# Kernel optimization log

Measured on AMD Instinct MI355X. Metric: run time of the kernel, lower is better.

## Reference

```python
import jax, jax.numpy as jnp
import numpy as np

D_MODEL = 256
D_INNER = 512   # expand=2 * d_model
D_STATE = 16
D_CONV = 4
DT_RANK = 16    # ceil(d_model/16)
N_BLOCKS = 5
BATCH = 8192
INPUT_DIM = 2048
NUM_CLASSES = 8


def setup_inputs() -> dict:
    key = jax.random.key(0)
    ks = jax.random.split(key, 10)
    rn = lambda k, shape, s: jax.random.normal(k, shape, jnp.float32) * s
    inp = {}
    inp['x'] = rn(ks[0], (BATCH, INPUT_DIM), 1.0)
    # preprocess Linear(input_dim, 256)
    inp['W_pre'] = rn(ks[1], (D_MODEL, INPUT_DIM), 0.02)
    inp['b_pre'] = jnp.zeros((D_MODEL,), jnp.float32)
    # per-block Mamba params, stacked over N_BLOCKS
    inp['in_proj_w'] = rn(ks[2], (N_BLOCKS, 2 * D_INNER, D_MODEL), 0.02)
    inp['conv_w'] = rn(ks[3], (N_BLOCKS, D_INNER, 1, D_CONV), 0.1)   # depthwise, groups=d_inner
    inp['conv_b'] = jnp.zeros((N_BLOCKS, D_INNER), jnp.float32)
    inp['x_proj_w'] = rn(ks[4], (N_BLOCKS, DT_RANK + 2 * D_STATE, D_INNER), 0.02)
    inp['dt_proj_w'] = rn(ks[5], (N_BLOCKS, D_INNER, DT_RANK), 0.1)
    inp['dt_proj_b'] = rn(ks[6], (N_BLOCKS, D_INNER), 0.1)
    # S4D-real init: A = 1..d_state, A_log = log(A)
    A = jnp.tile(jnp.arange(1, D_STATE + 1, dtype=jnp.float32)[None, None, :], (N_BLOCKS, D_INNER, 1))
    inp['A_log'] = jnp.log(A)
    inp['D'] = jnp.ones((N_BLOCKS, D_INNER), jnp.float32)
    inp['out_proj_w'] = rn(ks[7], (N_BLOCKS, D_MODEL, D_INNER), 0.02)
    inp['ln_g'] = jnp.ones((D_MODEL,), jnp.float32)
    inp['ln_b'] = jnp.zeros((D_MODEL,), jnp.float32)
    inp['W_cls'] = rn(ks[8], (NUM_CLASSES, D_MODEL), 0.02)
    inp['b_cls'] = jnp.zeros((NUM_CLASSES,), jnp.float32)
    return inp


def _mamba(x, in_w, cw, cb, xw, dtw, dtb, Alog, Dp, ow):
    # x: (B, L, d_model)
    B, L, _ = x.shape
    xz = jnp.einsum('bld,ed->ble', x, in_w)            # (B, L, 2*d_inner)
    xi, z = jnp.split(xz, 2, axis=-1)
    # causal depthwise conv1d over the sequence axis
    xt = xi.transpose(0, 2, 1)                         # (B, d_inner, L)
    xc = jax.lax.conv_general_dilated(
        xt, cw, window_strides=(1,), padding=[(D_CONV - 1, 0)],
        dimension_numbers=('NCH', 'OIH', 'NCH'), feature_group_count=D_INNER)
    xi = jax.nn.silu((xc + cb[None, :, None]).transpose(0, 2, 1))   # (B, L, d_inner)
    xdbl = jnp.einsum('bld,ed->ble', xi, xw)           # (B, L, dt_rank + 2*d_state)
    dt, Bm, Cm = jnp.split(xdbl, [DT_RANK, DT_RANK + D_STATE], axis=-1)
    dt = jax.nn.softplus(jnp.einsum('blr,dr->bld', dt, dtw) + dtb)  # (B, L, d_inner)
    A = -jnp.exp(Alog)                                  # (d_inner, d_state)
    dA = jnp.exp(dt[..., None] * A)                     # (B, L, d_inner, d_state)
    dBx = dt[..., None] * Bm[:, :, None, :] * xi[..., None]

    def step(h, t):
        dA_t, dBx_t, C_t = t
        h = dA_t * h + dBx_t                            # (B, d_inner, d_state)
        return h, jnp.einsum('bds,bs->bd', h, C_t)

    h0 = jnp.zeros((B, D_INNER, D_STATE), x.dtype)
    _, ys = jax.lax.scan(step, h0, (dA.swapaxes(0, 1), dBx.swapaxes(0, 1), Cm.swapaxes(0, 1)))
    y = ys.swapaxes(0, 1) + xi * Dp                     # (B, L, d_inner)
    y = y * jax.nn.silu(z)
    return jnp.einsum('bld,ed->ble', y, ow)             # (B, L, d_model)


def reference(x, W_pre, b_pre, in_proj_w, conv_w, conv_b, x_proj_w, dt_proj_w,
              dt_proj_b, A_log, D, out_proj_w, ln_g, ln_b, W_cls, b_cls):
    # dropout is identity in eval mode
    h = (x @ W_pre.T + b_pre)[:, None, :]               # (B, 1, 256)
    for i in range(N_BLOCKS):
        h = h + _mamba(h, in_proj_w[i], conv_w[i], conv_b[i], x_proj_w[i],
                       dt_proj_w[i], dt_proj_b[i], A_log[i], D[i], out_proj_w[i])
    mu = h.mean(-1, keepdims=True)
    var = ((h - mu) ** 2).mean(-1, keepdims=True)
    hn = (h - mu) * jax.lax.rsqrt(var + 1e-5) * ln_g + ln_b
    return hn[:, 0, :] @ W_cls.T + b_cls                # (B, num_classes)
```

## Files before the change

### kernel.cpp

```cpp
#include <hip/hip_runtime.h>
#include <hip/hip_bf16.h>

typedef __attribute__((ext_vector_type(8))) short bf16x8;
typedef __attribute__((ext_vector_type(4))) short s16x4;
typedef __attribute__((ext_vector_type(4))) float f32x4;
typedef __attribute__((ext_vector_type(4))) float float4v;

static __device__ __forceinline__ unsigned short f2b(float f) {
  unsigned int u = __builtin_bit_cast(unsigned int, f);
  u += 0x7fffu + ((u >> 16) & 1u);
  return (unsigned short)(u >> 16);
}
static __device__ __forceinline__ float b2f(unsigned short s) {
  unsigned int u = ((unsigned int)s) << 16;
  return __builtin_bit_cast(float, u);
}
static __device__ __forceinline__ float fsilu(float x) {
  float e = __builtin_amdgcn_exp2f(-1.44269504f * x);
  return x * __builtin_amdgcn_rcpf(1.f + e);
}
static __device__ __forceinline__ float fsoftplus(float a) {
  if (a > 20.f) return a;
  float t = __builtin_amdgcn_exp2f(1.44269504f * a);
  return 0.69314718f * __builtin_amdgcn_logf(1.f + t);
}
static __device__ __forceinline__ void gl16(const void* g, void* l) {
  __builtin_amdgcn_global_load_lds(
      (const __attribute__((address_space(1))) unsigned int*)g,
      (__attribute__((address_space(3))) unsigned int*)l, 16, 0, 0);
}
template <int N>
static __device__ __forceinline__ void waitv() {
  if constexpr (N == 0) asm volatile("s_waitcnt vmcnt(0)" ::: "memory");
  else if constexpr (N == 2) asm volatile("s_waitcnt vmcnt(2)" ::: "memory");
  else if constexpr (N == 4) asm volatile("s_waitcnt vmcnt(4)" ::: "memory");
  else if constexpr (N == 6) asm volatile("s_waitcnt vmcnt(6)" ::: "memory");
  else if constexpr (N == 8) asm volatile("s_waitcnt vmcnt(8)" ::: "memory");
}
static __device__ __forceinline__ void lgkm_bar() {
  asm volatile("s_waitcnt lgkmcnt(0)" ::: "memory");
  __builtin_amdgcn_s_barrier();
}

template <int TM, int TN>
__global__ __launch_bounds__(256) void gemm_pl(
    const unsigned short* __restrict__ A, const unsigned short* __restrict__ W,
    int N, int K, int GY,
    const float* __restrict__ p0, float* __restrict__ of,
    unsigned short* __restrict__ ob) {
  constexpr int FM = TM / 32, FN = TN / 32;
  constexpr int IA = TM / 64, IW = TN / 64;
  constexpr int LPT = IA + IW;
  __shared__ __align__(16) unsigned short As[4][TM * 32];
  __shared__ __align__(16) unsigned short Ws[4][TN * 32];

  const int t = threadIdx.x, lane = t & 63, wave = t >> 6;
  const int lr = lane & 15;
  const int q = gridDim.x >> 3;
  const int s = (blockIdx.x & 7) * q + (blockIdx.x >> 3);
  const int bm = (s / GY) * TM, bn = (s % GY) * TN;
  const int wr = (wave >> 1) * (TM / 2), wc = (wave & 1) * (TN / 2);

  f32x4 acc[FM][FN];
#pragma unroll
  for (int i = 0; i < FM; ++i)
#pragma unroll
    for (int j = 0; j < FN; ++j) acc[i][j] = (f32x4){0.f, 0.f, 0.f, 0.f};

  const unsigned short* agB =
      A + (long)(bm + wave * (TM / 4) + (lane >> 2)) * K +
      ((lane & 3) ^ ((lane >> 3) & 3)) * 8;
  const unsigned short* wgB =
      W + (long)(bn + wave * (TN / 4) + (lane >> 2)) * K +
      ((lane & 3) ^ ((lane >> 3) & 3)) * 8;

  auto STAGE = [&](int k0, int b) {
#pragma unroll
    for (int j = 0; j < IA; ++j)
      gl16(agB + k0 + (long)j * 16 * K, &As[b][(wave * (TM / 4) + j * 16) * 32]);
#pragma unroll
    for (int j = 0; j < IW; ++j)
      gl16(wgB + k0 + (long)j * 16 * K, &Ws[b][(wave * (TN / 4) + j * 16) * 32]);
  };

  auto COMPUTE = [&](int b) {
    bf16x8 af[FM], bg[FN];
    const int sw = ((lane >> 4) ^ ((lane >> 1) & 3)) * 8;
#pragma unroll
    for (int m = 0; m < FM; ++m)
      af[m] = *(const bf16x8*)&As[b][(wr + m * 16 + lr) * 32 + sw];
#pragma unroll
    for (int n = 0; n < FN; ++n)
      bg[n] = *(const bf16x8*)&Ws[b][(wc + n * 16 + lr) * 32 + sw];
    __builtin_amdgcn_s_setprio(1);
#pragma unroll
    for (int m = 0; m < FM; ++m)
#pragma unroll
      for (int n = 0; n < FN; ++n)
        acc[m][n] = __builtin_amdgcn_mfma_f32_16x16x32_bf16(af[m], bg[n],
                                                            acc[m][n], 0, 0, 0);
    __builtin_amdgcn_s_setprio(0);
  };

  const int NT = K >> 5;
  STAGE(0, 0);
  STAGE(32, 1);
  for (int tt = 0; tt < NT; ++tt) {
    if (tt + 2 < NT) {
      STAGE((tt + 2) << 5, (tt + 2) & 3);
      waitv<2 * LPT>();
    } else if (tt + 1 < NT) {
      waitv<LPT>();
    } else {
      waitv<0>();
    }
    __builtin_amdgcn_s_barrier();
    COMPUTE(tt & 3);
    __builtin_amdgcn_sched_barrier(0);
  }

  const int m0 = bm + wr + (lane >> 4) * 4;
  const int n0 = bn + wc + lr;
#pragma unroll
  for (int mi = 0; mi < FM; ++mi)
#pragma unroll
    for (int ni = 0; ni < FN; ++ni) {
      const int n = n0 + ni * 16;
#pragma unroll
      for (int r = 0; r < 4; ++r) {
        const int m = m0 + mi * 16 + r;
        float v = acc[mi][ni][r] + p0[n];
        of[(long)m * N + n] = v;
        ob[(long)m * N + n] = f2b(v);
      }
    }
}

__global__ __launch_bounds__(512) void mamba5(
    const unsigned short* __restrict__ hb0, const float* __restrict__ h0,
    const unsigned short* __restrict__ inwb,
    const unsigned short* __restrict__ xwpb,
    const unsigned short* __restrict__ dtwpb,
    const unsigned short* __restrict__ owb,
    const float* __restrict__ conv_b, const float* __restrict__ dt_b,
    const float* __restrict__ Dp, float* __restrict__ hout) {
  __shared__ __align__(16) unsigned short SMEM[81216];
  unsigned short* XiL = SMEM;
  unsigned short* SzL = SMEM + 16384;
  unsigned short* Ring = SMEM + 32768;
  unsigned short* HLr = SMEM + 65536;
  float* Dxl = (float*)(SMEM + 73728);
  float* BCl = (float*)(SMEM + 78080);
  float* Par = (float*)(SMEM + 78144);

  const int t = threadIdx.x, lane = t & 63, w = t >> 6;
  const int lr = lane & 15, lg = lane >> 4;
  const int bm = blockIdx.x * 32;
  const int fm = w & 1, fn = w >> 1;
  const int arow = fm * 16 + lr;
  const int br = fn * 16 + lr;
  const int m0 = fm * 16 + lg * 4;

#pragma unroll
  for (int j = 0; j < 2; ++j) {
    const int i = w * 2 + j;
    const int row = 2 * i + (lane >> 5);
    const int c = (lane & 31) ^ (row & 7);
    gl16(hb0 + (long)(bm + row) * 256 + c * 8, HLr + i * 512);
  }
  float hres[4][4];
#pragma unroll
  for (int ng = 0; ng < 4; ++ng)
#pragma unroll
    for (int r = 0; r < 4; ++r)
      hres[ng][r] = h0[(long)(bm + m0 + r) * 256 + ng * 64 + fn * 16 + lr];
  waitv<0>();
  __builtin_amdgcn_s_barrier();

  for (int blk = 0; blk < 5; ++blk) {
    const unsigned short* inw = inwb + (long)blk * 1024 * 256;
    const unsigned short* xwp = xwpb + (long)blk * 64 * 512;
    const unsigned short* dtwp = dtwpb + (long)blk * 512 * 32;
    const unsigned short* ow = owb + (long)blk * 256 * 512;
    const float* cbv = conv_b + blk * 512;
    const float* dtbv = dt_b + blk * 512;
    const float* Dv = Dp + blk * 512;

    auto STAGE1 = [&](int tt, int slot) {
      const int nt = tt >> 1, kh = tt & 1;
#pragma unroll
      for (int j = 0; j < 2; ++j) {
        const int u = w * 2 + j;
        const int row = 4 * u + (lane >> 4);
        const int c = (lane & 15) ^ (row & 7);
        gl16(inw + (long)(nt * 64 + row) * 256 + kh * 128 + c * 8,
             Ring + slot * 8192 + u * 512);
      }
    };
    if (w < 6) {
      const float* ps = (w < 2) ? cbv + (w & 1) * 256
                      : (w < 4) ? dtbv + (w & 1) * 256
                                : Dv + (w & 1) * 256;
      gl16(ps + lane * 4, (unsigned short*)Par + w * 512);
    }
    STAGE1(0, 0); STAGE1(1, 1); STAGE1(2, 2);
    f32x4 acc1 = {0.f, 0.f, 0.f, 0.f};
    for (int tt = 0; tt < 32; ++tt) {
      if (tt + 2 < 32) waitv<4>();
      else if (tt + 1 < 32) waitv<2>();
      else waitv<0>();
      __builtin_amdgcn_s_barrier();
      if (tt + 3 < 32) STAGE1(tt + 3, (tt + 3) & 3);
      __builtin_amdgcn_sched_barrier(0);
      const int nt = tt >> 1, kh = tt & 1;
      const int c = nt * 64 + fn * 16 + lr;
      if (kh == 0) {
        const float cb0 = (c < 512) ? Par[c] : 0.f;
        acc1 = (f32x4){cb0, cb0, cb0, cb0};
      }
      const unsigned short* Bs = Ring + (tt & 3) * 8192;
      {
        bf16x8 af[4], bg[4];
#pragma unroll
        for (int kc = 0; kc < 4; ++kc) {
          af[kc] = *(const bf16x8*)
              &HLr[arow * 256 + ((((kh * 4 + kc) * 4 + lg) ^ (arow & 7)) * 8)];
          bg[kc] = *(const bf16x8*)
              &Bs[br * 128 + (((kc * 4 + lg) ^ (br & 7)) * 8)];
        }
        __builtin_amdgcn_s_setprio(1);
#pragma unroll
        for (int kc = 0; kc < 4; ++kc)
          acc1 = __builtin_amdgcn_mfma_f32_16x16x32_bf16(af[kc], bg[kc], acc1,
                                                         0, 0, 0);
        __builtin_amdgcn_s_setprio(0);
      }
      if (kh == 1) {
        if (c < 512) {
#pragma unroll
          for (int r = 0; r < 4; ++r) {
            const int row = m0 + r;
            XiL[row * 512 + (((c >> 3) ^ (row & 7)) * 8) + (c & 7)] =
                f2b(fsilu(acc1[r]));
          }
        } else {
#pragma unroll
          for (int r = 0; r < 4; ++r)
            SzL[(m0 + r) * 512 + (c - 512)] = f2b(fsilu(acc1[r]));
        }
      }
      __builtin_amdgcn_sched_barrier(0);
    }
    lgkm_bar();

#pragma unroll
    for (int j = 0; j < 8; ++j) {
      const int i = w * 8 + j;
      gl16(xwp + (long)i * 512 + (lane ^ (i & 7)) * 8, Ring + i * 512);
    }
    waitv<0>();
    __builtin_amdgcn_s_barrier();
    {
      f32x4 a2 = {0.f, 0.f, 0.f, 0.f};
      bf16x8 af, bg;
      __builtin_amdgcn_s_setprio(1);
#pragma unroll
      for (int kc = 0; kc < 16; ++kc) {
        af = *(const bf16x8*)
            &XiL[arow * 512 + (((kc * 4 + lg) ^ (arow & 7)) * 8)];
        bg = *(const bf16x8*)
            &Ring[br * 512 + (((kc * 4 + lg) ^ (br & 7)) * 8)];
        a2 = __builtin_amdgcn_mfma_f32_16x16x32_bf16(af, bg, a2, 0, 0, 0);
      }
      __builtin_amdgcn_s_setprio(0);
#pragma unroll
      for (int r = 0; r < 4; ++r) Dxl[(m0 + r) * 68 + fn * 16 + lr] = a2[r];
    }
    lgkm_bar();

#pragma unroll
    for (int j = 0; j < 4; ++j) {
      const int u = w * 4 + j;
      const int row = u * 16 + (lane >> 2);
      const int c = (lane & 3) ^ (row & 3);
      gl16(dtwp + (long)row * 32 + c * 8, Ring + u * 512);
    }
    if (t < 32) {
      float bc = 0.f;
      const float* dx = &Dxl[t * 68];
#pragma unroll
      for (int s2 = 0; s2 < 16; ++s2) bc += dx[16 + s2] * dx[32 + s2];
      BCl[t] = bc;
    }
    bf16x8 afdt;
    {
      const float* dx = &Dxl[arow * 68 + lg * 8];
#pragma unroll
      for (int e = 0; e < 8; ++e) afdt[e] = (short)f2b(dx[e]);
    }
    waitv<0>();
    lgkm_bar();

#pragma unroll
    for (int tt = 0; tt < 8; ++tt) {
      const int d = tt * 64 + fn * 16 + lr;
      bf16x8 bg = *(const bf16x8*)&Ring[d * 32 + ((lg ^ (d & 3)) * 8)];
      f32x4 da = __builtin_amdgcn_mfma_f32_16x16x32_bf16(
          afdt, bg, (f32x4){0.f, 0.f, 0.f, 0.f}, 0, 0, 0);
      const float dbv = Par[512 + d], dvv = Par[1024 + d];
#pragma unroll
      for (int r = 0; r < 4; ++r) {
        const int row = m0 + r;
        const float dtv = fsoftplus(da[r] + dbv);
        const int xoff = row * 512 + (((d >> 3) ^ (row & 7)) * 8) + (d & 7);
        const float y = b2f(XiL[xoff]) * (dtv * BCl[row] + dvv) *
                        b2f(SzL[row * 512 + d]);
        XiL[xoff] = f2b(y);
      }
    }
    lgkm_bar();

    auto STAGE5 = [&](int tt, int slot) {
      const int ng = tt >> 2, kq = tt & 3;
#pragma unroll
      for (int j = 0; j < 2; ++j) {
        const int u = w * 2 + j;
        const int row = u * 4 + (lane >> 4);
        const int c = (lane & 15) ^ (row & 7);
        gl16(ow + (long)(ng * 64 + row) * 512 + kq * 128 + c * 8,
             Ring + slot * 8192 + u * 512);
      }
    };
    STAGE5(0, 0); STAGE5(1, 1); STAGE5(2, 2);
    f32x4 acc5 = {0.f, 0.f, 0.f, 0.f};
    for (int tt = 0; tt < 16; ++tt) {
      if (tt + 2 < 16) waitv<4>();
      else if (tt + 1 < 16) waitv<2>();
      else waitv<0>();
      __builtin_amdgcn_s_barrier();
      if (tt + 3 < 16) STAGE5(tt + 3, (tt + 3) & 3);
      __builtin_amdgcn_sched_barrier(0);
      const int ng = tt >> 2, kq = tt & 3;
      if (kq == 0) acc5 = (f32x4){0.f, 0.f, 0.f, 0.f};
      const unsigned short* Bs = Ring + (tt & 3) * 8192;
      {
        bf16x8 af[4], bg[4];
#pragma unroll
        for (int kc = 0; kc < 4; ++kc) {
          af[kc] = *(const bf16x8*)
              &XiL[arow * 512 + (((kq * 16 + kc * 4 + lg) ^ (arow & 7)) * 8)];
          bg[kc] = *(const bf16x8*)
              &Bs[br * 128 + (((kc * 4 + lg) ^ (br & 7)) * 8)];
        }
        __builtin_amdgcn_s_setprio(1);
#pragma unroll
        for (int kc = 0; kc < 4; ++kc)
          acc5 = __builtin_amdgcn_mfma_f32_16x16x32_bf16(af[kc], bg[kc], acc5,
                                                         0, 0, 0);
        __builtin_amdgcn_s_setprio(0);
      }
      if (kq == 3) {
        const int col = ng * 64 + fn * 16 + lr;
#pragma unroll
        for (int r = 0; r < 4; ++r) {
          const int row = m0 + r;
          const float v = acc5[r] + hres[ng][r];
          hres[ng][r] = v;
          HLr[row * 256 + (((col >> 3) ^ (row & 7)) * 8) + (col & 7)] = f2b(v);
        }
      }
      __builtin_amdgcn_sched_barrier(0);
    }
    lgkm_bar();
  }

#pragma unroll
  for (int ng = 0; ng < 4; ++ng)
#pragma unroll
    for (int r = 0; r < 4; ++r)
      hout[(long)(bm + m0 + r) * 256 + ng * 64 + fn * 16 + lr] = hres[ng][r];
}

__global__ __launch_bounds__(256) void castx(const float* __restrict__ s,
                                             unsigned short* __restrict__ d) {
  const int n4 = (8192 * 2048) / 4;
  for (int i = blockIdx.x * 256 + threadIdx.x; i < n4; i += gridDim.x * 256) {
    float4v v = ((const float4v*)s)[i];
    s16x4 o;
    o[0] = (short)f2b(v[0]); o[1] = (short)f2b(v[1]);
    o[2] = (short)f2b(v[2]); o[3] = (short)f2b(v[3]);
    ((s16x4*)d)[i] = o;
  }
}

__global__ __launch_bounds__(256) void precast(
    const float* __restrict__ wpre, const float* __restrict__ inw,
    const float* __restrict__ ow, const float* __restrict__ xw,
    const float* __restrict__ dtw, const float* __restrict__ cw,
    unsigned short* __restrict__ wpreb, unsigned short* __restrict__ inwb,
    unsigned short* __restrict__ owb, unsigned short* __restrict__ xwpb,
    unsigned short* __restrict__ dtwpb) {
  const int S0 = 524288;
  const int S1 = S0 + 1310720;
  const int S2 = S1 + 655360;
  const int S3 = S2 + 163840;
  const int S4 = S3 + 81920;
  int i4 = (blockIdx.x * 256 + threadIdx.x) * 4;
  if (i4 >= S4) return;
  float4v v = {0.f, 0.f, 0.f, 0.f};
  unsigned short* dst;
  if (i4 < S0) {
    v = *(const float4v*)(wpre + i4);
    dst = wpreb + i4;
  } else if (i4 < S1) {
    int o = i4 - S0;
    v = *(const float4v*)(inw + o);
    int b = o >> 18, row = (o >> 8) & 1023;
    if (row < 512) {
      float c3 = cw[(b * 512 + row) * 4 + 3];
      v[0] *= c3; v[1] *= c3; v[2] *= c3; v[3] *= c3;
    }
    dst = inwb + o;
  } else if (i4 < S2) {
    int o = i4 - S1;
    v = *(const float4v*)(ow + o);
    dst = owb + o;
  } else if (i4 < S3) {
    int o = i4 - S2;
    dst = xwpb + o;
    int k = o & 511, j = (o >> 9) & 63, b = o >> 15;
    if (j < 48) v = *(const float4v*)(xw + ((long)(b * 48 + j)) * 512 + k);
  } else {
    int o = i4 - S3;
    dst = dtwpb + o;
    int k = o & 31, dd = o >> 5;
    if (k < 16) v = *(const float4v*)(dtw + (long)dd * 16 + k);
  }
  s16x4 sv;
  sv[0] = (short)f2b(v[0]); sv[1] = (short)f2b(v[1]);
  sv[2] = (short)f2b(v[2]); sv[3] = (short)f2b(v[3]);
  *(s16x4*)dst = sv;
}

__global__ __launch_bounds__(256) void final_ln_cls(
    const float* __restrict__ h, const float* __restrict__ g,
    const float* __restrict__ be, const float* __restrict__ Wc,
    const float* __restrict__ bc, float* __restrict__ out) {
  const int wave = threadIdx.x >> 6, lane = threadIdx.x & 63;
  const int row = blockIdx.x * 4 + wave;
  const float4v* hr = (const float4v*)(h + (long)row * 256);
  float4v v = hr[lane];
  float s = v[0] + v[1] + v[2] + v[3];
#pragma unroll
  for (int o = 32; o; o >>= 1) s += __shfl_xor(s, o);
  const float mu = s * (1.f / 256.f);
  float d0 = v[0] - mu, d1 = v[1] - mu, d2 = v[2] - mu, d3 = v[3] - mu;
  float qq = d0 * d0 + d1 * d1 + d2 * d2 + d3 * d3;
#pragma unroll
  for (int o = 32; o; o >>= 1) qq += __shfl_xor(qq, o);
  const float rs = rsqrtf(qq * (1.f / 256.f) + 1e-5f);
  const float4v gv = ((const float4v*)g)[lane];
  const float4v bv = ((const float4v*)be)[lane];
  float hn[4];
  hn[0] = d0 * rs * gv[0] + bv[0];
  hn[1] = d1 * rs * gv[1] + bv[1];
  hn[2] = d2 * rs * gv[2] + bv[2];
  hn[3] = d3 * rs * gv[3] + bv[3];
  float lg[8];
#pragma unroll
  for (int o = 0; o < 8; ++o) {
    const float4v wv = ((const float4v*)(Wc + o * 256))[lane];
    float p = hn[0] * wv[0] + hn[1] * wv[1] + hn[2] * wv[2] + hn[3] * wv[3];
#pragma unroll
    for (int x = 32; x; x >>= 1) p += __shfl_xor(p, x);
    lg[o] = p;
  }
  if (lane == 0) {
#pragma unroll
    for (int o = 0; o < 8; ++o) out[(long)row * 8 + o] = lg[o] + bc[o];
  }
}

extern "C" void kernel_launch(void* const* d_in, const int* in_sizes, int n_in,
                              void* d_out, int out_size, void* d_ws,
                              size_t ws_size, hipStream_t stream) {
  const float* x      = (const float*)d_in[0];
  const float* W_pre  = (const float*)d_in[1];
  const float* b_pre  = (const float*)d_in[2];
  const float* in_w   = (const float*)d_in[3];
  const float* conv_w = (const float*)d_in[4];
  const float* conv_b = (const float*)d_in[5];
  const float* x_w    = (const float*)d_in[6];
  const float* dt_w   = (const float*)d_in[7];
  const float* dt_b   = (const float*)d_in[8];
  const float* Dp     = (const float*)d_in[10];
  const float* out_w  = (const float*)d_in[11];
  const float* ln_g   = (const float*)d_in[12];
  const float* ln_b   = (const float*)d_in[13];
  const float* W_cls  = (const float*)d_in[14];
  const float* b_cls  = (const float*)d_in[15];
  float* out = (float*)d_out;

  char* w = (char*)d_ws;
  unsigned short* wpreb = (unsigned short*)w; w += 256 * 2048 * 2;
  unsigned short* inwb  = (unsigned short*)w; w += 5 * 1024 * 256 * 2;
  unsigned short* xwpb  = (unsigned short*)w; w += 5 * 64 * 512 * 2;
  unsigned short* owb   = (unsigned short*)w; w += 5 * 256 * 512 * 2;
  unsigned short* dtwpb = (unsigned short*)w; w += 5 * 512 * 32 * 2;
  float*          h     = (float*)w;          w += 8192 * 256 * 4;
  unsigned short* hb    = (unsigned short*)w; w += 8192 * 256 * 2;
  unsigned short* xb    = (unsigned short*)w; w += 8192 * 2048 * 2;

  precast<<<2672, 256, 0, stream>>>(W_pre, in_w, out_w, x_w, dt_w, conv_w,
                                    wpreb, inwb, owb, xwpb, dtwpb);
  castx<<<2048, 256, 0, stream>>>(x, xb);

  gemm_pl<128, 64><<<256, 256, 0, stream>>>(
      xb, wpreb, 256, 2048, 4, b_pre, h, hb);

  mamba5<<<256, 512, 0, stream>>>(hb, h, inwb, xwpb, dtwpb, owb,
                                  conv_b, dt_b, Dp, h);

  final_ln_cls<<<2048, 256, 0, stream>>>(h, ln_g, ln_b, W_cls, b_cls, out);
}
```

Baseline: 220.7 us.

## Retile in_proj and out_proj GEMMs to 2x2 MFMA fragments per wave with larger stages

Each wave now computes a 32x32 register tile (2x2 MFMA fragments) over full N-chunks of 256 columns instead of one 16x16 fragment. This gives fragment reuse, since each A and B fragment loaded from LDS feeds two MFMAs. Weight staging moves from a 4-slot ring of 64x128 tiles with a prefetch depth of 3 to a double buffer of 256x64 tiles with a full vmcnt(0) wait each step. This cuts LDS reads and barrier count per MFMA, but trades away deeper prefetch and raises register pressure from the extra accumulators.

```diff
diff --git a/kernel.cpp b/kernel.cpp
--- a/kernel.cpp
+++ b/kernel.cpp
@@ -33,6 +33,7 @@
 static __device__ __forceinline__ void waitv() {
   if constexpr (N == 0) asm volatile("s_waitcnt vmcnt(0)" ::: "memory");
   else if constexpr (N == 2) asm volatile("s_waitcnt vmcnt(2)" ::: "memory");
+  else if constexpr (N == 3) asm volatile("s_waitcnt vmcnt(3)" ::: "memory");
   else if constexpr (N == 4) asm volatile("s_waitcnt vmcnt(4)" ::: "memory");
   else if constexpr (N == 6) asm volatile("s_waitcnt vmcnt(6)" ::: "memory");
   else if constexpr (N == 8) asm volatile("s_waitcnt vmcnt(8)" ::: "memory");
@@ -156,10 +157,10 @@
   const int t = threadIdx.x, lane = t & 63, w = t >> 6;
   const int lr = lane & 15, lg = lane >> 4;
   const int bm = blockIdx.x * 32;
-  const int fm = w & 1, fn = w >> 1;
-  const int arow = fm * 16 + lr;
-  const int br = fn * 16 + lr;
-  const int m0 = fm * 16 + lg * 4;
+  const int m04 = lg * 4;
+  const int srow8 = lane >> 3;
+  const int sc = (lane & 7) ^ srow8;
+  const int wc32 = w * 32;
 
 #pragma unroll
   for (int j = 0; j < 2; ++j) {
@@ -168,12 +169,15 @@
     const int c = (lane & 31) ^ (row & 7);
     gl16(hb0 + (long)(bm + row) * 256 + c * 8, HLr + i * 512);
   }
-  float hres[4][4];
-#pragma unroll
-  for (int ng = 0; ng < 4; ++ng)
-#pragma unroll
-    for (int r = 0; r < 4; ++r)
-      hres[ng][r] = h0[(long)(bm + m0 + r) * 256 + ng * 64 + fn * 16 + lr];
+  float hres[2][2][4];
+#pragma unroll
+  for (int fm = 0; fm < 2; ++fm)
+#pragma unroll
+    for (int n = 0; n < 2; ++n)
+#pragma unroll
+      for (int r = 0; r < 4; ++r)
+        hres[fm][n][r] =
+            h0[(long)(bm + fm * 16 + m04 + r) * 256 + wc32 + n * 16 + lr];
   waitv<0>();
   __builtin_amdgcn_s_barrier();
 
@@ -186,15 +190,12 @@
     const float* dtbv = dt_b + blk * 512;
     const float* Dv = Dp + blk * 512;
 
-    auto STAGE1 = [&](int tt, int slot) {
-      const int nt = tt >> 1, kh = tt & 1;
-#pragma unroll
-      for (int j = 0; j < 2; ++j) {
-        const int u = w * 2 + j;
-        const int row = 4 * u + (lane >> 4);
-        const int c = (lane & 15) ^ (row & 7);
-        gl16(inw + (long)(nt * 64 + row) * 256 + kh * 128 + c * 8,
-             Ring + slot * 8192 + u * 512);
+    auto STAGE1 = [&](int p, int qq, int slot) {
+#pragma unroll
+      for (int j = 0; j < 4; ++j) {
+        const int u = w * 4 + j;
+        gl16(inw + (long)(p * 256 + u * 8 + srow8) * 256 + qq * 64 + sc * 8,
+             Ring + slot * 16384 + u * 512);
       }
     };
     if (w < 6) {
@@ -203,53 +204,69 @@
                                 : Dv + (w & 1) * 256;
       gl16(ps + lane * 4, (unsigned short*)Par + w * 512);
     }
-    STAGE1(0, 0); STAGE1(1, 1); STAGE1(2, 2);
-    f32x4 acc1 = {0.f, 0.f, 0.f, 0.f};
-    for (int tt = 0; tt < 32; ++tt) {
-      if (tt + 2 < 32) waitv<4>();
-      else if (tt + 1 < 32) waitv<2>();
-      else waitv<0>();
-      __builtin_amdgcn_s_barrier();
-      if (tt + 3 < 32) STAGE1(tt + 3, (tt + 3) & 3);
-      __builtin_amdgcn_sched_barrier(0);
-      const int nt = tt >> 1, kh = tt & 1;
-      const int c = nt * 64 + fn * 16 + lr;
-      if (kh == 0) {
-        const float cb0 = (c < 512) ? Par[c] : 0.f;
-        acc1 = (f32x4){cb0, cb0, cb0, cb0};
-      }
-      const unsigned short* Bs = Ring + (tt & 3) * 8192;
-      {
-        bf16x8 af[4], bg[4];
-#pragma unroll
-        for (int kc = 0; kc < 4; ++kc) {
-          af[kc] = *(const bf16x8*)
-              &HLr[arow * 256 + ((((kh * 4 + kc) * 4 + lg) ^ (arow & 7)) * 8)];
-          bg[kc] = *(const bf16x8*)
-              &Bs[br * 128 + (((kc * 4 + lg) ^ (br & 7)) * 8)];
+    STAGE1(0, 0, 0);
+    f32x4 acc1[2][2];
+#pragma unroll
+    for (int p = 0; p < 4; ++p) {
+#pragma unroll
+      for (int qq = 0; qq < 4; ++qq) {
+        waitv<0>();
+        __builtin_amdgcn_s_barrier();
+        if (qq < 3) STAGE1(p, qq + 1, (qq + 1) & 1);
+        else if (p < 3) STAGE1(p + 1, 0, 0);
+        __builtin_amdgcn_sched_barrier(0);
+        if (qq == 0) {
+#pragma unroll
+          for (int n = 0; n < 2; ++n) {
+            const int c = p * 256 + wc32 + n * 16 + lr;
+            const float cb = (p < 2) ? Par[c] : 0.f;
+            acc1[0][n] = (f32x4){cb, cb, cb, cb};
+            acc1[1][n] = acc1[0][n];
+          }
+        }
+        const unsigned short* Bs = Ring + (qq & 1) * 16384;
+        bf16x8 af[2][2], bg[2][2];
+#pragma unroll
+        for (int kc = 0; kc < 2; ++kc) {
+          const int e = ((kc * 4 + lg) ^ (lr & 7)) * 8;
+#pragma unroll
+          for (int fm = 0; fm < 2; ++fm)
+            af[fm][kc] =
+                *(const bf16x8*)&HLr[(fm * 16 + lr) * 256 + qq * 64 + e];
+#pragma unroll
+          for (int n = 0; n < 2; ++n)
+            bg[n][kc] = *(const bf16x8*)&Bs[(wc32 + n * 16 + lr) * 64 + e];
         }
         __builtin_amdgcn_s_setprio(1);
 #pragma unroll
-        for (int kc = 0; kc < 4; ++kc)
-          acc1 = __builtin_amdgcn_mfma_f32_16x16x32_bf16(af[kc], bg[kc], acc1,
-                                                         0, 0, 0);
+        for (int kc = 0; kc < 2; ++kc)
+#pragma unroll
+          for (int fm = 0; fm < 2; ++fm)
+#pragma unroll
+            for (int n = 0; n < 2; ++n)
+              acc1[fm][n] = __builtin_amdgcn_mfma_f32_16x16x32_bf16(
+                  af[fm][kc], bg[n][kc], acc1[fm][n], 0, 0, 0);
         __builtin_amdgcn_s_setprio(0);
-      }
-      if (kh == 1) {
-        if (c < 512) {
-#pragma unroll
-          for (int r = 0; r < 4; ++r) {
-            const int row = m0 + r;
-            XiL[row * 512 + (((c >> 3) ^ (row & 7)) * 8) + (c & 7)] =
-                f2b(fsilu(acc1[r]));
-          }
-        } else {
-#pragma unroll
-          for (int r = 0; r < 4; ++r)
-            SzL[(m0 + r) * 512 + (c - 512)] = f2b(fsilu(acc1[r]));
+        if (qq == 3) {
+#pragma unroll
+          for (int fm = 0; fm < 2; ++fm)
+#pragma unroll
+            for (int n = 0; n < 2; ++n) {
+              const int c = p * 256 + wc32 + n * 16 + lr;
+#pragma unroll
+              for (int r = 0; r < 4; ++r) {
+                const int row = fm * 16 + m04 + r;
+                const float v = fsilu(acc1[fm][n][r]);
+                if (p < 2)
+                  XiL[row * 512 + (((c >> 3) ^ (row & 7)) * 8) + (c & 7)] =
+                      f2b(v);
+                else
+                  SzL[row * 512 + (c - 512)] = f2b(v);
+              }
+            }
         }
-      }
-      __builtin_amdgcn_sched_barrier(0);
+        __builtin_amdgcn_sched_barrier(0);
+      }
     }
     lgkm_bar();
 
@@ -261,20 +278,22 @@
     waitv<0>();
     __builtin_amdgcn_s_barrier();
     {
+      const int fm2 = w & 1, fn2 = w >> 1;
+      const int ar = fm2 * 16 + lr, rb = fn2 * 16 + lr;
       f32x4 a2 = {0.f, 0.f, 0.f, 0.f};
-      bf16x8 af, bg;
       __builtin_amdgcn_s_setprio(1);
 #pragma unroll
       for (int kc = 0; kc < 16; ++kc) {
-        af = *(const bf16x8*)
-            &XiL[arow * 512 + (((kc * 4 + lg) ^ (arow & 7)) * 8)];
-        bg = *(const bf16x8*)
-            &Ring[br * 512 + (((kc * 4 + lg) ^ (br & 7)) * 8)];
+        bf16x8 af = *(const bf16x8*)
+            &XiL[ar * 512 + (((kc * 4 + lg) ^ (lr & 7)) * 8)];
+        bf16x8 bg = *(const bf16x8*)
+            &Ring[rb * 512 + (((kc * 4 + lg) ^ (lr & 7)) * 8)];
         a2 = __builtin_amdgcn_mfma_f32_16x16x32_bf16(af, bg, a2, 0, 0, 0);
       }
       __builtin_amdgcn_s_setprio(0);
 #pragma unroll
-      for (int r = 0; r < 4; ++r) Dxl[(m0 + r) * 68 + fn * 16 + lr] = a2[r];
+      for (int r = 0; r < 4; ++r)
+        Dxl[(fm2 * 16 + m04 + r) * 68 + fn2 * 16 + lr] = a2[r];
     }
     lgkm_bar();
 
@@ -294,91 +313,104 @@
     }
     bf16x8 afdt;
     {
-      const float* dx = &Dxl[arow * 68 + lg * 8];
+      const float* dx = &Dxl[((w & 1) * 16 + lr) * 68 + lg * 8];
 #pragma unroll
       for (int e = 0; e < 8; ++e) afdt[e] = (short)f2b(dx[e]);
     }
     waitv<0>();
     lgkm_bar();
 
+    {
+      const int fn4 = w >> 1, m04b = (w & 1) * 16 + m04;
+#pragma unroll
+      for (int tt = 0; tt < 8; ++tt) {
+        const int d = tt * 64 + fn4 * 16 + lr;
+        bf16x8 bg = *(const bf16x8*)&Ring[d * 32 + ((lg ^ (d & 3)) * 8)];
+        f32x4 da = __builtin_amdgcn_mfma_f32_16x16x32_bf16(
+            afdt, bg, (f32x4){0.f, 0.f, 0.f, 0.f}, 0, 0, 0);
+        const float dbv = Par[512 + d], dvv = Par[1024 + d];
+#pragma unroll
+        for (int r = 0; r < 4; ++r) {
+          const int row = m04b + r;
+          const float dtv = fsoftplus(da[r] + dbv);
+          const int xoff = row * 512 + (((d >> 3) ^ (row & 7)) * 8) + (d & 7);
+          const float y = b2f(XiL[xoff]) * (dtv * BCl[row] + dvv) *
+                          b2f(SzL[row * 512 + d]);
+          XiL[xoff] = f2b(y);
+        }
+      }
+    }
+    lgkm_bar();
+
+    auto STAGE5 = [&](int tt, int slot) {
+#pragma unroll
+      for (int j = 0; j < 4; ++j) {
+        const int u = w * 4 + j;
+        gl16(ow + (long)(u * 8 + srow8) * 512 + tt * 64 + sc * 8,
+             Ring + slot * 16384 + u * 512);
+      }
+    };
+    STAGE5(0, 0);
+    f32x4 acc5[2][2];
+#pragma unroll
+    for (int fm = 0; fm < 2; ++fm)
+#pragma unroll
+      for (int n = 0; n < 2; ++n) acc5[fm][n] = (f32x4){0.f, 0.f, 0.f, 0.f};
 #pragma unroll
     for (int tt = 0; tt < 8; ++tt) {
-      const int d = tt * 64 + fn * 16 + lr;
-      bf16x8 bg = *(const bf16x8*)&Ring[d * 32 + ((lg ^ (d & 3)) * 8)];
-      f32x4 da = __builtin_amdgcn_mfma_f32_16x16x32_bf16(
-          afdt, bg, (f32x4){0.f, 0.f, 0.f, 0.f}, 0, 0, 0);
-      const float dbv = Par[512 + d], dvv = Par[1024 + d];
-#pragma unroll
-      for (int r = 0; r < 4; ++r) {
-        const int row = m0 + r;
-        const float dtv = fsoftplus(da[r] + dbv);
-        const int xoff = row * 512 + (((d >> 3) ^ (row & 7)) * 8) + (d & 7);
-        const float y = b2f(XiL[xoff]) * (dtv * BCl[row] + dvv) *
-                        b2f(SzL[row * 512 + d]);
-        XiL[xoff] = f2b(y);
-      }
-    }
-    lgkm_bar();
-
-    auto STAGE5 = [&](int tt, int slot) {
-      const int ng = tt >> 2, kq = tt & 3;
-#pragma unroll
-      for (int j = 0; j < 2; ++j) {
-        const int u = w * 2 + j;
-        const int row = u * 4 + (lane >> 4);
-        const int c = (lane & 15) ^ (row & 7);
-        gl16(ow + (long)(ng * 64 + row) * 512 + kq * 128 + c * 8,
-             Ring + slot * 8192 + u * 512);
-      }
-    };
-    STAGE5(0, 0); STAGE5(1, 1); STAGE5(2, 2);
-    f32x4 acc5 = {0.f, 0.f, 0.f, 0.f};
-    for (int tt = 0; tt < 16; ++tt) {
-      if (tt + 2 < 16) waitv<4>();
-      else if (tt + 1 < 16) waitv<2>();
-      else waitv<0>();
+      waitv<0>();
       __builtin_amdgcn_s_barrier();
-      if (tt + 3 < 16) STAGE5(tt + 3, (tt + 3) & 3);
+      if (tt < 7) STAGE5(tt + 1, (tt + 1) & 1);
       __builtin_amdgcn_sched_barrier(0);
-      const int ng = tt >> 2, kq = tt & 3;
-      if (kq == 0) acc5 = (f32x4){0.f, 0.f, 0.f, 0.f};
-      const unsigned short* Bs = Ring + (tt & 3) * 8192;
-      {
-        bf16x8 af[4], bg[4];
-#pragma unroll
-        for (int kc = 0; kc < 4; ++kc) {
-          af[kc] = *(const bf16x8*)
-              &XiL[arow * 512 + (((kq * 16 + kc * 4 + lg) ^ (arow & 7)) * 8)];
-          bg[kc] = *(const bf16x8*)
-              &Bs[br * 128 + (((kc * 4 + lg) ^ (br & 7)) * 8)];
-        }
-        __builtin_amdgcn_s_setprio(1);
-#pragma unroll
-        for (int kc = 0; kc < 4; ++kc)
-          acc5 = __builtin_amdgcn_mfma_f32_16x16x32_bf16(af[kc], bg[kc], acc5,
-                                                         0, 0, 0);
-        __builtin_amdgcn_s_setprio(0);
-      }
-      if (kq == 3) {
-        const int col = ng * 64 + fn * 16 + lr;
+      const unsigned short* Bs = Ring + (tt & 1) * 16384;
+      bf16x8 af[2][2], bg[2][2];
+#pragma unroll
+      for (int kc = 0; kc < 2; ++kc) {
+        const int e = ((kc * 4 + lg) ^ (lr & 7)) * 8;
+#pragma unroll
+        for (int fm = 0; fm < 2; ++fm)
+          af[fm][kc] =
+              *(const bf16x8*)&XiL[(fm * 16 + lr) * 512 + tt * 64 + e];
+#pragma unroll
+        for (int n = 0; n < 2; ++n)
+          bg[n][kc] = *(const bf16x8*)&Bs[(wc32 + n * 16 + lr) * 64 + e];
+      }
+      __builtin_amdgcn_s_setprio(1);
+#pragma unroll
+      for (int kc = 0; kc < 2; ++kc)
+#pragma unroll
+        for (int fm = 0; fm < 2; ++fm)
+#pragma unroll
+          for (int n = 0; n < 2; ++n)
+            acc5[fm][n] = __builtin_amdgcn_mfma_f32_16x16x32_bf16(
+                af[fm][kc], bg[n][kc], acc5[fm][n], 0, 0, 0);
+      __builtin_amdgcn_s_setprio(0);
+      __builtin_amdgcn_sched_barrier(0);
+    }
+#pragma unroll
+    for (int fm = 0; fm < 2; ++fm)
+#pragma unroll
+      for (int n = 0; n < 2; ++n) {
+        const int col = wc32 + n * 16 + lr;
 #pragma unroll
         for (int r = 0; r < 4; ++r) {
-          const int row = m0 + r;
-          const float v = acc5[r] + hres[ng][r];
-          hres[ng][r] = v;
+          const int row = fm * 16 + m04 + r;
+          const float v = acc5[fm][n][r] + hres[fm][n][r];
+          hres[fm][n][r] = v;
           HLr[row * 256 + (((col >> 3) ^ (row & 7)) * 8) + (col & 7)] = f2b(v);
         }
       }
-      __builtin_amdgcn_sched_barrier(0);
-    }
     lgkm_bar();
   }
 
 #pragma unroll
-  for (int ng = 0; ng < 4; ++ng)
-#pragma unroll
-    for (int r = 0; r < 4; ++r)
-      hout[(long)(bm + m0 + r) * 256 + ng * 64 + fn * 16 + lr] = hres[ng][r];
+  for (int fm = 0; fm < 2; ++fm)
+#pragma unroll
+    for (int n = 0; n < 2; ++n)
+#pragma unroll
+      for (int r = 0; r < 4; ++r)
+        hout[(long)(bm + fm * 16 + m04 + r) * 256 + wc32 + n * 16 + lr] =
+            hres[fm][n][r];
 }
 
 __global__ __launch_bounds__(256) void castx(const float* __restrict__ s,
```

Result: slower. 243.5 us (+10.3%).
